# Kernel tuning notes

Hardware: AMD Instinct MI355X
Metric: run time of the kernel (lower is better)

The kernel has to match this reference:

```python
import jax, jax.numpy as jnp
import numpy as np

N, G, E, D, H = 50000, 1000, 400000, 128, 256


def _sample_negatives(edge_index, batch, rng):
    # Vectorized equivalent of the torch per-edge loop: for each positive edge,
    # draw a dst in the same graph as src, excluding src itself and src's
    # existing neighbors, via 8 rounds of rejection sampling.
    src = edge_index[0]
    counts = np.bincount(batch, minlength=G)
    starts = np.concatenate([[0], np.cumsum(counts)[:-1]])
    g = batch[src]
    edge_keys = np.unique(edge_index[0].astype(np.int64) * N + edge_index[1])
    dst = src.copy()
    valid = np.zeros(E, dtype=bool)
    for _ in range(8):
        cand = starts[g] + rng.integers(0, counts[g])
        ok = (cand != src) & ~np.isin(src.astype(np.int64) * N + cand, edge_keys)
        take = ok & ~valid
        dst = np.where(take, cand, dst)
        valid |= ok
    fallback = starts[g] + (src - starts[g] + 1) % counts[g]  # deterministic in-graph node != src (when graph>1)
    dst = np.where(valid, dst, fallback)
    return np.stack([src, dst]).astype(np.int64)


def setup_inputs() -> dict:
    rng = np.random.default_rng(0)
    batch = np.sort(rng.integers(0, G, size=N)).astype(np.int64)  # contiguous graph ids
    counts = np.bincount(batch, minlength=G)
    starts = np.concatenate([[0], np.cumsum(counts)[:-1]])
    src = rng.integers(0, N, size=E)
    gsrc = batch[src]
    dst = starts[gsrc] + rng.integers(0, counts[gsrc])  # same-graph positive edges
    edge_index = np.stack([src, dst]).astype(np.int64)
    neg_edge_index = _sample_negatives(edge_index, batch, rng)

    key = jax.random.key(0)
    ks = jax.random.split(key, 4)
    x = jax.random.normal(ks[0], (N, D), jnp.float32)
    w1 = jax.random.normal(ks[1], (2 * D, H), jnp.float32) / np.sqrt(2 * D)
    w2 = jax.random.normal(ks[2], (H, H // 2), jnp.float32) / np.sqrt(H)
    w3 = jax.random.normal(ks[3], (H // 2, 1), jnp.float32) / np.sqrt(H // 2)
    return {
        "x": x,
        "edge_index": jnp.asarray(edge_index),
        "batch": jnp.asarray(batch),
        "neg_edge_index": jnp.asarray(neg_edge_index),
        "w1": w1, "b1": jnp.zeros((H,), jnp.float32),
        "g1": jnp.ones((H,), jnp.float32), "be1": jnp.zeros((H,), jnp.float32),
        "w2": w2, "b2": jnp.zeros((H // 2,), jnp.float32),
        "g2": jnp.ones((H // 2,), jnp.float32), "be2": jnp.zeros((H // 2,), jnp.float32),
        "w3": w3, "b3": jnp.zeros((1,), jnp.float32),
    }


def _layernorm(h, g, b, eps=1e-5):
    m = jnp.mean(h, axis=-1, keepdims=True)
    v = jnp.mean(jnp.square(h - m), axis=-1, keepdims=True)
    return (h - m) * jax.lax.rsqrt(v + eps) * g + b


def _edge_mlp(feat, w1, b1, g1, be1, w2, b2, g2, be2, w3, b3):
    h = jax.nn.relu(_layernorm(feat @ w1 + b1, g1, be1))
    h = jax.nn.relu(_layernorm(h @ w2 + b2, g2, be2))
    return jax.nn.sigmoid(h @ w3 + b3)


def reference(x, edge_index, batch, neg_edge_index, w1, b1, g1, be1, w2, b2, g2, be2, w3, b3):
    # batch is consumed by the (setup-time) negative sampler; kept for signature fidelity.
    all_idx = jnp.concatenate([edge_index, neg_edge_index], axis=1)  # [2, 2E]
    feat = jnp.concatenate([x[all_idx[0]], x[all_idx[1]]], axis=-1)  # [2E, 2D]
    pred = _edge_mlp(feat, w1, b1, g1, be1, w2, b2, g2, be2, w3, b3)  # [2E, 1]
    num_pos = edge_index.shape[1]
    num_neg = neg_edge_index.shape[1]
    labels = jnp.concatenate(
        [jnp.ones((num_pos, 1), pred.dtype), jnp.zeros((num_neg, 1), pred.dtype)], axis=0
    )
    return pred, labels
```

## Files before the change

### kernel.cpp

```cpp
#include <hip/hip_runtime.h>
#include <math.h>
#include <stdint.h>

#define NN    50000
#define EPOS  400000
#define ROWS  800000
#define DIM   128
#define D2    256
#define H1C   256
#define H2C   128
#define MT    64
#define NTH   512

typedef __bf16 bf16;
typedef __bf16 bf16x8 __attribute__((ext_vector_type(8)));
typedef __bf16 bf16x4 __attribute__((ext_vector_type(4)));
typedef float  f32x4  __attribute__((ext_vector_type(4)));

#define XB_N   (NN*DIM)
#define W1F_E  XB_N
#define W1F_N  (H1C*D2)
#define W2F_E  (XB_N + W1F_N)
#define W2F_N  (H2C*H1C)
#define WS_NEEDED ((size_t)(XB_N + W1F_N + W2F_N) * 2)

#define AOFF  0
#define SCR   32768
#define SCR2  34816
#define CFOFF 35840
#define SMEM_BYTES 40960

__device__ __forceinline__ void gll16(const void* g, void* l) {
    __builtin_amdgcn_global_load_lds(
        (const __attribute__((address_space(1))) void*)g,
        (__attribute__((address_space(3))) void*)l, 16, 0, 0);
}

__global__ void preconv(const float* __restrict__ x, const float* __restrict__ w1,
                        const float* __restrict__ w2, bf16* __restrict__ ws,
                        float* __restrict__ out) {
    int gi = blockIdx.x * 256 + threadIdx.x;
    if (gi < ROWS) out[ROWS + gi] = (gi < EPOS) ? 1.f : 0.f;
    int i = gi;
    if (i < XB_N) { ws[i] = (bf16)x[i]; return; }
    i -= XB_N;
    if (i < W1F_N) {
        int j = i & 7, l = (i >> 3) & 63, ct = i >> 9;
        int c = ct >> 4, t = ct & 15;
        int n = t * 16 + (l & 15);
        int k = c * 32 + (l >> 4) * 8 + j;
        ws[W1F_E + i] = (bf16)w1[k * H1C + n];
        return;
    }
    i -= W1F_N;
    if (i < W2F_N) {
        int j = i & 7, l = (i >> 3) & 63, ct = i >> 9;
        int c = ct >> 3, t = ct & 7;
        int n = t * 16 + (l & 15);
        int k = c * 32 + (l >> 4) * 8 + j;
        ws[W2F_E + i] = (bf16)w2[k * H2C + n];
    }
}

__global__ __launch_bounds__(NTH, 4) void lp_mfma11(
    const bf16* __restrict__ xb, const bf16* __restrict__ w1f, const bf16* __restrict__ w2f,
    const int*  __restrict__ ei, const int* __restrict__ nei,
    const float* __restrict__ b1, const float* __restrict__ g1, const float* __restrict__ be1,
    const float* __restrict__ b2, const float* __restrict__ g2, const float* __restrict__ be2,
    const float* __restrict__ w3, const float* __restrict__ b3,
    float* __restrict__ out)
{
    extern __shared__ char smem[];
    const int tid  = threadIdx.x;
    const int lane = tid & 63;
    const int w    = tid >> 6;
    const int wm   = w >> 2;
    const int wn   = w & 3;
    const int gr0  = blockIdx.x * MT;
    const int l15  = lane & 15;
    const int l4   = lane >> 4;

    #pragma unroll
    for (int ii = 0; ii < 4; ++ii) {
        const int i = w * 4 + ii;
        uint32_t doff = (uint32_t)(i << 10) + (uint32_t)(lane << 4);
        uint32_t loff = doff ^ (((doff >> 9) & 7u) << 4);
        int row = loff >> 9;
        int inb = loff & 511;
        int gr  = gr0 + row;
        int node;
        if (inb < 256) { node = (gr < EPOS) ? ei[gr]        : nei[gr - EPOS]; }
        else           { node = (gr < EPOS) ? ei[EPOS + gr] : nei[gr]; inb -= 256; }
        gll16((const char*)xb + (((size_t)node) << 8) + inb, smem + AOFF + (i << 10));
    }

    for (int i = tid; i < 1280; i += NTH) {
        float v;
        if      (i < 256)  v = b1[i];
        else if (i < 512)  v = g1[i - 256];
        else if (i < 768)  v = be1[i - 512];
        else if (i < 896)  v = b2[i - 768];
        else if (i < 1024) v = g2[i - 896];
        else if (i < 1152) v = be2[i - 1024];
        else               v = w3[i - 1152];
        *(float*)(smem + CFOFF + i * 4) = v;
    }

    uint32_t abase[2], asw[2];
    #pragma unroll
    for (int mi = 0; mi < 2; ++mi) {
        int row = (wm << 5) + (mi << 4) + l15;
        abase[mi] = (uint32_t)row << 9;
        asw[mi]   = (uint32_t)(row & 7) << 4;
    }
    const uint32_t koff  = (uint32_t)l4 << 4;
    const uint32_t c1off = ((uint32_t)wn << 8) + ((uint32_t)l4 << 4);
    const uint32_t c2off = ((uint32_t)wn << 7) + ((uint32_t)l4 << 4);

    __syncthreads();

    f32x4 acc1s[2][4];
    #pragma unroll
    for (int ni = 0; ni < 4; ++ni) {
        f32x4 bias = *(const f32x4*)(smem + CFOFF + c1off + (ni << 6));
        acc1s[0][ni] = bias; acc1s[1][ni] = bias;
    }
    const bf16* bp1 = w1f + (wn << 11) + (lane << 3);
    #pragma unroll
    for (int c = 0; c < 8; ++c) {
        bf16x8 af[2];
        #pragma unroll
        for (int mi = 0; mi < 2; ++mi)
            af[mi] = *(const bf16x8*)(smem + AOFF + ((abase[mi] + ((uint32_t)c << 6) + koff) ^ asw[mi]));
        #pragma unroll
        for (int ni = 0; ni < 4; ++ni) {
            bf16x8 bfr = *(const bf16x8*)(bp1 + (c << 13) + (ni << 9));
            #pragma unroll
            for (int mi = 0; mi < 2; ++mi)
                acc1s[mi][ni] = __builtin_amdgcn_mfma_f32_16x16x32_bf16(
                    bfr, af[mi], acc1s[mi][ni], 0, 0, 0);
        }
    }

    #pragma unroll
    for (int mi = 0; mi < 2; ++mi) {
        float s1 = 0.f, s2 = 0.f;
        #pragma unroll
        for (int ni = 0; ni < 4; ++ni)
            #pragma unroll
            for (int j = 0; j < 4; ++j) {
                float v = acc1s[mi][ni][j];
                s1 += v; s2 += v * v;
            }
        s1 += __shfl_xor(s1, 16); s1 += __shfl_xor(s1, 32);
        s2 += __shfl_xor(s2, 16); s2 += __shfl_xor(s2, 32);
        if (l4 == 0) {
            int row = (wm << 5) + (mi << 4) + l15;
            *(float2*)(smem + SCR + (row << 5) + (wn << 3)) = make_float2(s1, s2);
        }
    }
    __syncthreads();

    #pragma unroll
    for (int mi = 0; mi < 2; ++mi) {
        int row = (wm << 5) + (mi << 4) + l15;
        f32x4 p0 = *(const f32x4*)(smem + SCR + (row << 5));
        f32x4 p1 = *(const f32x4*)(smem + SCR + (row << 5) + 16);
        float s1 = p0[0] + p0[2] + p1[0] + p1[2];
        float s2 = p0[1] + p0[3] + p1[1] + p1[3];
        float mean = s1 * (1.f / 256.f);
        float var  = s2 * (1.f / 256.f) - mean * mean;
        float rstd = rsqrtf(var + 1e-5f);
        #pragma unroll
        for (int ni = 0; ni < 4; ++ni) {
            f32x4 gv  = *(const f32x4*)(smem + CFOFF + 1024 + c1off + (ni << 6));
            f32x4 bev = *(const f32x4*)(smem + CFOFF + 2048 + c1off + (ni << 6));
            bf16x4 hb;
            #pragma unroll
            for (int j = 0; j < 4; ++j) {
                float h = (acc1s[mi][ni][j] - mean) * rstd * gv[j] + bev[j];
                hb[j] = (bf16)fmaxf(h, 0.f);
            }
            uint32_t byte = ((uint32_t)row << 9) + ((uint32_t)wn << 7) + ((uint32_t)ni << 5) + ((uint32_t)l4 << 3);
            byte ^= ((byte >> 9) & 7u) << 4;
            *(bf16x4*)(smem + AOFF + byte) = hb;
        }
    }
    __syncthreads();

    f32x4 acc2s[2][2];
    #pragma unroll
    for (int ni = 0; ni < 2; ++ni) {
        f32x4 bias = *(const f32x4*)(smem + CFOFF + 3072 + c2off + (ni << 6));
        acc2s[0][ni] = bias; acc2s[1][ni] = bias;
    }
    const bf16* bp2 = w2f + (wn << 10) + (lane << 3);
    #pragma unroll
    for (int c = 0; c < 8; ++c) {
        bf16x8 a2[2];
        #pragma unroll
        for (int mi = 0; mi < 2; ++mi)
            a2[mi] = *(const bf16x8*)(smem + AOFF + ((abase[mi] + ((uint32_t)c << 6) + koff) ^ asw[mi]));
        #pragma unroll
        for (int ni = 0; ni < 2; ++ni) {
            bf16x8 b2r = *(const bf16x8*)(bp2 + (c << 12) + (ni << 9));
            #pragma unroll
            for (int mi = 0; mi < 2; ++mi)
                acc2s[mi][ni] = __builtin_amdgcn_mfma_f32_16x16x32_bf16(
                    b2r, a2[mi], acc2s[mi][ni], 0, 0, 0);
        }
    }

    #pragma unroll
    for (int mi = 0; mi < 2; ++mi) {
        float s1 = 0.f, s2 = 0.f;
        #pragma unroll
        for (int ni = 0; ni < 2; ++ni)
            #pragma unroll
            for (int j = 0; j < 4; ++j) {
                float v = acc2s[mi][ni][j];
                s1 += v; s2 += v * v;
            }
        s1 += __shfl_xor(s1, 16); s1 += __shfl_xor(s1, 32);
        s2 += __shfl_xor(s2, 16); s2 += __shfl_xor(s2, 32);
        if (l4 == 0) {
            int row = (wm << 5) + (mi << 4) + l15;
            *(float2*)(smem + SCR + (row << 5) + (wn << 3)) = make_float2(s1, s2);
        }
    }
    __syncthreads();

    #pragma unroll
    for (int mi = 0; mi < 2; ++mi) {
        int row = (wm << 5) + (mi << 4) + l15;
        f32x4 p0 = *(const f32x4*)(smem + SCR + (row << 5));
        f32x4 p1 = *(const f32x4*)(smem + SCR + (row << 5) + 16);
        float s1 = p0[0] + p0[2] + p1[0] + p1[2];
        float s2 = p0[1] + p0[3] + p1[1] + p1[3];
        float mean = s1 * (1.f / 128.f);
        float var  = s2 * (1.f / 128.f) - mean * mean;
        float rstd = rsqrtf(var + 1e-5f);
        float zp = 0.f;
        #pragma unroll
        for (int ni = 0; ni < 2; ++ni) {
            f32x4 gv  = *(const f32x4*)(smem + CFOFF + 3584 + c2off + (ni << 6));
            f32x4 bev = *(const f32x4*)(smem + CFOFF + 4096 + c2off + (ni << 6));
            f32x4 wv  = *(const f32x4*)(smem + CFOFF + 4608 + c2off + (ni << 6));
            #pragma unroll
            for (int j = 0; j < 4; ++j) {
                float h = (acc2s[mi][ni][j] - mean) * rstd * gv[j] + bev[j];
                h = fmaxf(h, 0.f);
                zp += h * wv[j];
            }
        }
        zp += __shfl_xor(zp, 16); zp += __shfl_xor(zp, 32);
        if (l4 == 0)
            *(float*)(smem + SCR2 + (row << 4) + (wn << 2)) = zp;
    }
    __syncthreads();

    if (wn == 0) {
        const float b3s = b3[0];
        #pragma unroll
        for (int mi = 0; mi < 2; ++mi) {
            int row = (wm << 5) + (mi << 4) + l15;
            if (l4 == 0) {
                f32x4 zv = *(const f32x4*)(smem + SCR2 + (row << 4));
                float z = zv[0] + zv[1] + zv[2] + zv[3] + b3s;
                out[gr0 + row] = 1.f / (1.f + expf(-z));
            }
        }
    }
}

#define TILE  32
#define PAD   264
__global__ __launch_bounds__(256, 4) void lp_fused(
    const float* __restrict__ x, const int* __restrict__ ei, const int* __restrict__ nei,
    const float* __restrict__ w1, const float* __restrict__ b1,
    const float* __restrict__ g1, const float* __restrict__ be1,
    const float* __restrict__ w2, const float* __restrict__ b2,
    const float* __restrict__ g2, const float* __restrict__ be2,
    const float* __restrict__ w3, const float* __restrict__ b3,
    float* __restrict__ out)
{
    __shared__ float lds[TILE][PAD];
    const int t = threadIdx.x, e = t >> 3, jg = t & 7;
    const int row = blockIdx.x * TILE + e;
    {
        int src, dst;
        if (row < EPOS) { src = ei[row];         dst = ei[EPOS + row]; }
        else            { src = nei[row - EPOS]; dst = nei[row]; }
        const float* base = (jg < 4) ? (x + src * DIM + jg * 32) : (x + dst * DIM + (jg - 4) * 32);
        const float4* b4 = (const float4*)base;
        #pragma unroll
        for (int s = 0; s < 8; ++s) *(float4*)&lds[e][jg * 32 + s * 4] = b4[s];
    }
    __syncthreads();
    float acc[32];
    #pragma unroll
    for (int i = 0; i < 32; ++i) acc[i] = 0.f;
    const int j0 = jg * 32;
    for (int k4 = 0; k4 < D2 / 4; ++k4) {
        float4 a4 = *(const float4*)&lds[e][k4 * 4];
        float av[4] = {a4.x, a4.y, a4.z, a4.w};
        #pragma unroll
        for (int kk = 0; kk < 4; ++kk) {
            const float a = av[kk];
            const float4* wr = (const float4*)(w1 + (k4 * 4 + kk) * H1C + j0);
            #pragma unroll
            for (int ii = 0; ii < 8; ++ii) {
                float4 wv = wr[ii];
                acc[ii*4+0] += a*wv.x; acc[ii*4+1] += a*wv.y; acc[ii*4+2] += a*wv.z; acc[ii*4+3] += a*wv.w;
            }
        }
    }
    float s1 = 0.f, s2 = 0.f;
    #pragma unroll
    for (int i = 0; i < 32; ++i) { float h = acc[i] + b1[j0+i]; acc[i] = h; s1 += h; s2 += h*h; }
    #pragma unroll
    for (int m = 1; m < 8; m <<= 1) { s1 += __shfl_xor(s1, m, 8); s2 += __shfl_xor(s2, m, 8); }
    float mean = s1 * (1.f/256.f), var = s2 * (1.f/256.f) - mean*mean, rstd = rsqrtf(var + 1e-5f);
    __syncthreads();
    #pragma unroll
    for (int i = 0; i < 32; ++i)
        lds[e][j0+i] = fmaxf((acc[i]-mean)*rstd*g1[j0+i]+be1[j0+i], 0.f);
    __syncthreads();
    float acc2[16];
    #pragma unroll
    for (int i = 0; i < 16; ++i) acc2[i] = 0.f;
    const int q0 = jg * 16;
    for (int k4 = 0; k4 < H1C / 4; ++k4) {
        float4 a4 = *(const float4*)&lds[e][k4 * 4];
        float av[4] = {a4.x, a4.y, a4.z, a4.w};
        #pragma unroll
        for (int kk = 0; kk < 4; ++kk) {
            const float a = av[kk];
            const float4* wr = (const float4*)(w2 + (k4 * 4 + kk) * H2C + q0);
            #pragma unroll
            for (int ii = 0; ii < 4; ++ii) {
                float4 wv = wr[ii];
                acc2[ii*4+0] += a*wv.x; acc2[ii*4+1] += a*wv.y; acc2[ii*4+2] += a*wv.z; acc2[ii*4+3] += a*wv.w;
            }
        }
    }
    s1 = 0.f; s2 = 0.f;
    #pragma unroll
    for (int i = 0; i < 16; ++i) { float h = acc2[i] + b2[q0+i]; acc2[i] = h; s1 += h; s2 += h*h; }
    #pragma unroll
    for (int m = 1; m < 8; m <<= 1) { s1 += __shfl_xor(s1, m, 8); s2 += __shfl_xor(s2, m, 8); }
    mean = s1 * (1.f/128.f); var = s2 * (1.f/128.f) - mean*mean; rstd = rsqrtf(var + 1e-5f);
    float zp = 0.f;
    #pragma unroll
    for (int i = 0; i < 16; ++i) {
        float h = fmaxf((acc2[i]-mean)*rstd*g2[q0+i]+be2[q0+i], 0.f);
        zp += h * w3[q0+i];
    }
    #pragma unroll
    for (int m = 1; m < 8; m <<= 1) zp += __shfl_xor(zp, m, 8);
    if (jg == 0) out[row] = 1.f / (1.f + expf(-(zp + b3[0])));
    if (jg == 1) out[ROWS + row] = (row < EPOS) ? 1.f : 0.f;
}

extern "C" void kernel_launch(void* const* d_in, const int* in_sizes, int n_in,
                              void* d_out, int out_size, void* d_ws, size_t ws_size,
                              hipStream_t stream) {
    const float* x   = (const float*)d_in[0];
    const int*   ei  = (const int*)d_in[1];
    const int*   nei = (const int*)d_in[3];
    const float* w1  = (const float*)d_in[4];
    const float* b1  = (const float*)d_in[5];
    const float* g1  = (const float*)d_in[6];
    const float* be1 = (const float*)d_in[7];
    const float* w2  = (const float*)d_in[8];
    const float* b2  = (const float*)d_in[9];
    const float* g2  = (const float*)d_in[10];
    const float* be2 = (const float*)d_in[11];
    const float* w3  = (const float*)d_in[12];
    const float* b3  = (const float*)d_in[13];
    float* out = (float*)d_out;

    if (ws_size >= WS_NEEDED) {
        bf16* ws = (bf16*)d_ws;
        const int total = XB_N + W1F_N + W2F_N;
        hipLaunchKernelGGL(preconv, dim3((total + 255) / 256), dim3(256), 0, stream,
                           x, w1, w2, ws, out);
        hipFuncSetAttribute((const void*)lp_mfma11,
                            hipFuncAttributeMaxDynamicSharedMemorySize, SMEM_BYTES);
        hipLaunchKernelGGL(lp_mfma11, dim3(ROWS / MT), dim3(NTH), SMEM_BYTES, stream,
                           ws, ws + W1F_E, ws + W2F_E, ei, nei,
                           b1, g1, be1, b2, g2, be2, w3, b3, out);
    } else {
        hipLaunchKernelGGL(lp_fused, dim3(ROWS / TILE), dim3(256), 0, stream,
                           x, ei, nei, w1, b1, g1, be1, w2, b2, g2, be2, w3, b3, out);
    }
}
```

Measured before the change: 270.0 us.

## Precompute per-node first-layer projections and gather them per edge

The first linear layer is split as x[src]@W1a + x[dst]@W1b. A new node_gemm kernel computes both halves for all 50k nodes once (Y of size N×512 in bf16). The edge kernel then gathers and adds the two 256-wide projections before LayerNorm, skipping the per-edge 256×256 GEMM. The cost is an extra kernel, a 51 MB bf16 intermediate, and doubled gather bytes per edge (1 KB vs 512 B). The path only runs when the workspace is large enough, otherwise it falls back to the old kernel.

```diff
diff --git a/kernel.cpp b/kernel.cpp
--- a/kernel.cpp
+++ b/kernel.cpp
@@ -18,23 +18,327 @@
 typedef float  f32x4  __attribute__((ext_vector_type(4)));
 
 #define XB_N   (NN*DIM)
-#define W1F_E  XB_N
-#define W1F_N  (H1C*D2)
-#define W2F_E  (XB_N + W1F_N)
+#define WAF_E  XB_N
+#define WAF_N  (128*512)
+#define W2F_E  (WAF_E + WAF_N)
 #define W2F_N  (H2C*H1C)
-#define WS_NEEDED ((size_t)(XB_N + W1F_N + W2F_N) * 2)
+#define Y_E    (W2F_E + W2F_N)
+#define Y_N    (NN*512)
+#define WS1_NEEDED ((size_t)(W2F_E + W2F_N) * 2)
+#define WS2_NEEDED ((size_t)(Y_E + Y_N) * 2)
+
+__device__ __forceinline__ void gll16(const void* g, void* l) {
+    __builtin_amdgcn_global_load_lds(
+        (const __attribute__((address_space(1))) void*)g,
+        (__attribute__((address_space(3))) void*)l, 16, 0, 0);
+}
+
+__global__ void preconv2(const float* __restrict__ x, const float* __restrict__ w1,
+                         const float* __restrict__ w2, bf16* __restrict__ ws,
+                         float* __restrict__ out) {
+    int gi = blockIdx.x * 256 + threadIdx.x;
+    if (gi < ROWS) out[ROWS + gi] = (gi < EPOS) ? 1.f : 0.f;
+    int i = gi;
+    if (i < XB_N) { ws[i] = (bf16)x[i]; return; }
+    i -= XB_N;
+    if (i < WAF_N) {
+        int j = i & 7, l = (i >> 3) & 63, ct = i >> 9;
+        int c = ct >> 5, t = ct & 31;
+        int np = t * 16 + (l & 15);
+        int k  = c * 32 + (l >> 4) * 8 + j;
+        float v = (np < 256) ? w1[k * H1C + np] : w1[(128 + k) * H1C + (np - 256)];
+        ws[WAF_E + i] = (bf16)v;
+        return;
+    }
+    i -= WAF_N;
+    if (i < W2F_N) {
+        int j = i & 7, l = (i >> 3) & 63, ct = i >> 9;
+        int c = ct >> 3, t = ct & 7;
+        int n = t * 16 + (l & 15);
+        int k = c * 32 + (l >> 4) * 8 + j;
+        ws[W2F_E + i] = (bf16)w2[k * H2C + n];
+    }
+}
+
+__global__ __launch_bounds__(512, 4) void node_gemm(
+    const bf16* __restrict__ xb, const bf16* __restrict__ waf,
+    const float* __restrict__ b1, bf16* __restrict__ Y)
+{
+    __shared__ char smem[16384];
+    const int tid  = threadIdx.x;
+    const int lane = tid & 63;
+    const int w    = tid >> 6;
+    const int wm   = w >> 2;
+    const int wn   = w & 3;
+    const int n0   = blockIdx.x * 64;
+    const int l15  = lane & 15;
+    const int l4   = lane >> 4;
+
+    #pragma unroll
+    for (int ii = 0; ii < 2; ++ii) {
+        const int i = w * 2 + ii;
+        uint32_t doff = (uint32_t)(i << 10) + (uint32_t)(lane << 4);
+        uint32_t loff = doff ^ (((doff >> 8) & 7u) << 4);
+        int row  = loff >> 8;
+        int inb  = loff & 255;
+        int node = n0 + row; if (node >= NN) node = NN - 1;
+        gll16((const char*)xb + ((size_t)node << 8) + inb, smem + (i << 10));
+    }
+    __syncthreads();
+
+    f32x4 acc[2][8] = {};
+    const bf16* bp = waf + (wn << 12) + (lane << 3);
+    uint32_t abase[2], asw[2];
+    #pragma unroll
+    for (int mi = 0; mi < 2; ++mi) {
+        int row = (wm << 5) + (mi << 4) + l15;
+        abase[mi] = (uint32_t)row << 8;
+        asw[mi]   = (uint32_t)(row & 7) << 4;
+    }
+    #pragma unroll
+    for (int c = 0; c < 4; ++c) {
+        bf16x8 af[2];
+        #pragma unroll
+        for (int mi = 0; mi < 2; ++mi)
+            af[mi] = *(const bf16x8*)(smem + ((abase[mi] + ((uint32_t)c << 6) + ((uint32_t)l4 << 4)) ^ asw[mi]));
+        #pragma unroll
+        for (int ni = 0; ni < 8; ++ni) {
+            bf16x8 bfr = *(const bf16x8*)(bp + (c << 14) + (ni << 9));
+            #pragma unroll
+            for (int mi = 0; mi < 2; ++mi)
+                acc[mi][ni] = __builtin_amdgcn_mfma_f32_16x16x32_bf16(
+                    bfr, af[mi], acc[mi][ni], 0, 0, 0);
+        }
+    }
+
+    #pragma unroll
+    for (int mi = 0; mi < 2; ++mi) {
+        int node = n0 + (wm << 5) + (mi << 4) + l15;
+        if (node >= NN) continue;
+        #pragma unroll
+        for (int ni = 0; ni < 8; ++ni) {
+            int col = (wn << 7) + (ni << 4) + (l4 << 2);
+            f32x4 a = acc[mi][ni];
+            if (wn < 2) {
+                f32x4 bv = *(const f32x4*)(b1 + col);
+                a[0] += bv[0]; a[1] += bv[1]; a[2] += bv[2]; a[3] += bv[3];
+            }
+            bf16x4 ob;
+            #pragma unroll
+            for (int j = 0; j < 4; ++j) ob[j] = (bf16)a[j];
+            *(bf16x4*)(Y + ((size_t)node << 9) + col) = ob;
+        }
+    }
+}
+
+#define SOFF  0
+#define DOFF  32768
+#define BSCR  65536
+#define BSCR2 67584
+#define BCF   68608
+#define BSMEM 72704
+
+__global__ __launch_bounds__(NTH, 4) void lp_edge(
+    const bf16* __restrict__ Y, const bf16* __restrict__ w2f,
+    const int*  __restrict__ ei, const int* __restrict__ nei,
+    const float* __restrict__ g1, const float* __restrict__ be1,
+    const float* __restrict__ b2, const float* __restrict__ g2, const float* __restrict__ be2,
+    const float* __restrict__ w3, const float* __restrict__ b3,
+    float* __restrict__ out)
+{
+    extern __shared__ char smem[];
+    const int tid  = threadIdx.x;
+    const int lane = tid & 63;
+    const int w    = tid >> 6;
+    const int wm   = w >> 2;
+    const int wn   = w & 3;
+    const int gr0  = blockIdx.x * MT;
+    const int l15  = lane & 15;
+    const int l4   = lane >> 4;
+
+    #pragma unroll
+    for (int ii = 0; ii < 8; ++ii) {
+        const int i = w * 8 + ii;
+        const int u = i & 31;
+        const int half = i >> 5;
+        uint32_t doff = (uint32_t)(u << 10) + (uint32_t)(lane << 4);
+        uint32_t loff = doff ^ (((doff >> 9) & 7u) << 4);
+        int row = loff >> 9;
+        int inb = loff & 511;
+        int gr  = gr0 + row;
+        int node = (half == 0) ? ((gr < EPOS) ? ei[gr]        : nei[gr - EPOS])
+                               : ((gr < EPOS) ? ei[EPOS + gr] : nei[gr]);
+        gll16((const char*)Y + ((size_t)node << 10) + (half << 9) + inb,
+              smem + (half ? DOFF : SOFF) + (u << 10));
+    }
+
+    for (int i = tid; i < 1024; i += NTH) {
+        float v;
+        if      (i < 256) v = g1[i];
+        else if (i < 512) v = be1[i - 256];
+        else if (i < 640) v = b2[i - 512];
+        else if (i < 768) v = g2[i - 640];
+        else if (i < 896) v = be2[i - 768];
+        else              v = w3[i - 896];
+        *(float*)(smem + BCF + i * 4) = v;
+    }
+
+    uint32_t abase[2], asw[2];
+    #pragma unroll
+    for (int mi = 0; mi < 2; ++mi) {
+        int row = (wm << 5) + (mi << 4) + l15;
+        abase[mi] = (uint32_t)row << 9;
+        asw[mi]   = (uint32_t)(row & 7) << 4;
+    }
+    const uint32_t koff  = (uint32_t)l4 << 4;
+    const uint32_t c1off = ((uint32_t)wn << 8) + ((uint32_t)l4 << 4);
+    const uint32_t c2off = ((uint32_t)wn << 7) + ((uint32_t)l4 << 4);
+
+    __syncthreads();
+
+    f32x4 pv[2][4];
+    #pragma unroll
+    for (int mi = 0; mi < 2; ++mi) {
+        float s1 = 0.f, s2 = 0.f;
+        int row = (wm << 5) + (mi << 4) + l15;
+        uint32_t rsw = (uint32_t)(row & 7) << 4;
+        #pragma unroll
+        for (int ni = 0; ni < 4; ++ni) {
+            uint32_t byte = (((uint32_t)row << 9) + ((uint32_t)wn << 7) + ((uint32_t)ni << 5) + ((uint32_t)l4 << 3)) ^ rsw;
+            bf16x4 sv = *(const bf16x4*)(smem + SOFF + byte);
+            bf16x4 dv = *(const bf16x4*)(smem + DOFF + byte);
+            f32x4 v;
+            #pragma unroll
+            for (int j = 0; j < 4; ++j) {
+                v[j] = (float)sv[j] + (float)dv[j];
+                s1 += v[j]; s2 += v[j] * v[j];
+            }
+            pv[mi][ni] = v;
+        }
+        s1 += __shfl_xor(s1, 16); s1 += __shfl_xor(s1, 32);
+        s2 += __shfl_xor(s2, 16); s2 += __shfl_xor(s2, 32);
+        if (l4 == 0)
+            *(float2*)(smem + BSCR + (row << 5) + (wn << 3)) = make_float2(s1, s2);
+    }
+    __syncthreads();
+
+    #pragma unroll
+    for (int mi = 0; mi < 2; ++mi) {
+        int row = (wm << 5) + (mi << 4) + l15;
+        f32x4 p0 = *(const f32x4*)(smem + BSCR + (row << 5));
+        f32x4 p1 = *(const f32x4*)(smem + BSCR + (row << 5) + 16);
+        float s1 = p0[0] + p0[2] + p1[0] + p1[2];
+        float s2 = p0[1] + p0[3] + p1[1] + p1[3];
+        float mean = s1 * (1.f / 256.f);
+        float var  = s2 * (1.f / 256.f) - mean * mean;
+        float rstd = rsqrtf(var + 1e-5f);
+        #pragma unroll
+        for (int ni = 0; ni < 4; ++ni) {
+            f32x4 gv  = *(const f32x4*)(smem + BCF + c1off + (ni << 6));
+            f32x4 bev = *(const f32x4*)(smem + BCF + 1024 + c1off + (ni << 6));
+            bf16x4 hb;
+            #pragma unroll
+            for (int j = 0; j < 4; ++j) {
+                float h = (pv[mi][ni][j] - mean) * rstd * gv[j] + bev[j];
+                hb[j] = (bf16)fmaxf(h, 0.f);
+            }
+            uint32_t byte = ((uint32_t)row << 9) + ((uint32_t)wn << 7) + ((uint32_t)ni << 5) + ((uint32_t)l4 << 3);
+            byte ^= ((byte >> 9) & 7u) << 4;
+            *(bf16x4*)(smem + SOFF + byte) = hb;
+        }
+    }
+    __syncthreads();
+
+    f32x4 acc2s[2][2];
+    #pragma unroll
+    for (int ni = 0; ni < 2; ++ni) {
+        f32x4 bias = *(const f32x4*)(smem + BCF + 2048 + c2off + (ni << 6));
+        acc2s[0][ni] = bias; acc2s[1][ni] = bias;
+    }
+    const bf16* bp2 = w2f + (wn << 10) + (lane << 3);
+    #pragma unroll
+    for (int c = 0; c < 8; ++c) {
+        bf16x8 a2[2];
+        #pragma unroll
+        for (int mi = 0; mi < 2; ++mi)
+            a2[mi] = *(const bf16x8*)(smem + SOFF + ((abase[mi] + ((uint32_t)c << 6) + koff) ^ asw[mi]));
+        #pragma unroll
+        for (int ni = 0; ni < 2; ++ni) {
+            bf16x8 b2r = *(const bf16x8*)(bp2 + (c << 12) + (ni << 9));
+            #pragma unroll
+            for (int mi = 0; mi < 2; ++mi)
+                acc2s[mi][ni] = __builtin_amdgcn_mfma_f32_16x16x32_bf16(
+                    b2r, a2[mi], acc2s[mi][ni], 0, 0, 0);
+        }
+    }
+
+    #pragma unroll
+    for (int mi = 0; mi < 2; ++mi) {
+        float s1 = 0.f, s2 = 0.f;
+        #pragma unroll
+        for (int ni = 0; ni < 2; ++ni)
+            #pragma unroll
+            for (int j = 0; j < 4; ++j) {
+                float v = acc2s[mi][ni][j];
+                s1 += v; s2 += v * v;
+            }
+        s1 += __shfl_xor(s1, 16); s1 += __shfl_xor(s1, 32);
+        s2 += __shfl_xor(s2, 16); s2 += __shfl_xor(s2, 32);
+        if (l4 == 0) {
+            int row = (wm << 5) + (mi << 4) + l15;
+            *(float2*)(smem + BSCR + (row << 5) + (wn << 3)) = make_float2(s1, s2);
+        }
+    }
+    __syncthreads();
+
+    #pragma unroll
+    for (int mi = 0; mi < 2; ++mi) {
+        int row = (wm << 5) + (mi << 4) + l15;
+        f32x4 p0 = *(const f32x4*)(smem + BSCR + (row << 5));
+        f32x4 p1 = *(const f32x4*)(smem + BSCR + (row << 5) + 16);
+        float s1 = p0[0] + p0[2] + p1[0] + p1[2];
+        float s2 = p0[1] + p0[3] + p1[1] + p1[3];
+        float mean = s1 * (1.f / 128.f);
+        float var  = s2 * (1.f / 128.f) - mean * mean;
+        float rstd = rsqrtf(var + 1e-5f);
+        float zp = 0.f;
+        #pragma unroll
+        for (int ni = 0; ni < 2; ++ni) {
+            f32x4 gv  = *(const f32x4*)(smem + BCF + 2560 + c2off + (ni << 6));
+            f32x4 bev = *(const f32x4*)(smem + BCF + 3072 + c2off + (ni << 6));
+            f32x4 wv  = *(const f32x4*)(smem + BCF + 3584 + c2off + (ni << 6));
+            #pragma unroll
+            for (int j = 0; j < 4; ++j) {
+                float h = (acc2s[mi][ni][j] - mean) * rstd * gv[j] + bev[j];
+                h = fmaxf(h, 0.f);
+                zp += h * wv[j];
+            }
+        }
+        zp += __shfl_xor(zp, 16); zp += __shfl_xor(zp, 32);
+        if (l4 == 0)
+            *(float*)(smem + BSCR2 + (row << 4) + (wn << 2)) = zp;
+    }
+    __syncthreads();
+
+    if (wn == 0) {
+        const float b3s = b3[0];
+        #pragma unroll
+        for (int mi = 0; mi < 2; ++mi) {
+            int row = (wm << 5) + (mi << 4) + l15;
+            if (l4 == 0) {
+                f32x4 zv = *(const f32x4*)(smem + BSCR2 + (row << 4));
+                float z = zv[0] + zv[1] + zv[2] + zv[3] + b3s;
+                out[gr0 + row] = 1.f / (1.f + expf(-z));
+            }
+        }
+    }
+}
 
 #define AOFF  0
 #define SCR   32768
 #define SCR2  34816
 #define CFOFF 35840
 #define SMEM_BYTES 40960
-
-__device__ __forceinline__ void gll16(const void* g, void* l) {
-    __builtin_amdgcn_global_load_lds(
-        (const __attribute__((address_space(1))) void*)g,
-        (__attribute__((address_space(3))) void*)l, 16, 0, 0);
-}
 
 __global__ void preconv(const float* __restrict__ x, const float* __restrict__ w1,
                         const float* __restrict__ w2, bf16* __restrict__ ws,
@@ -44,15 +348,15 @@
     int i = gi;
     if (i < XB_N) { ws[i] = (bf16)x[i]; return; }
     i -= XB_N;
-    if (i < W1F_N) {
+    if (i < WAF_N) {
         int j = i & 7, l = (i >> 3) & 63, ct = i >> 9;
         int c = ct >> 4, t = ct & 15;
         int n = t * 16 + (l & 15);
         int k = c * 32 + (l >> 4) * 8 + j;
-        ws[W1F_E + i] = (bf16)w1[k * H1C + n];
+        ws[WAF_E + i] = (bf16)w1[k * H1C + n];
         return;
     }
-    i -= W1F_N;
+    i -= WAF_N;
     if (i < W2F_N) {
         int j = i & 7, l = (i >> 3) & 63, ct = i >> 9;
         int c = ct >> 3, t = ct & 7;
@@ -93,7 +397,6 @@
         else           { node = (gr < EPOS) ? ei[EPOS + gr] : nei[gr]; inb -= 256; }
         gll16((const char*)xb + (((size_t)node) << 8) + inb, smem + AOFF + (i << 10));
     }
-
     for (int i = tid; i < 1280; i += NTH) {
         float v;
         if      (i < 256)  v = b1[i];
@@ -105,7 +408,6 @@
         else               v = w3[i - 1152];
         *(float*)(smem + CFOFF + i * 4) = v;
     }
-
     uint32_t abase[2], asw[2];
     #pragma unroll
     for (int mi = 0; mi < 2; ++mi) {
@@ -116,7 +418,6 @@
     const uint32_t koff  = (uint32_t)l4 << 4;
     const uint32_t c1off = ((uint32_t)wn << 8) + ((uint32_t)l4 << 4);
     const uint32_t c2off = ((uint32_t)wn << 7) + ((uint32_t)l4 << 4);
-
     __syncthreads();
 
     f32x4 acc1s[2][4];
@@ -141,7 +442,6 @@
                     bfr, af[mi], acc1s[mi][ni], 0, 0, 0);
         }
     }
-
     #pragma unroll
     for (int mi = 0; mi < 2; ++mi) {
         float s1 = 0.f, s2 = 0.f;
@@ -160,7 +460,6 @@
         }
     }
     __syncthreads();
-
     #pragma unroll
     for (int mi = 0; mi < 2; ++mi) {
         int row = (wm << 5) + (mi << 4) + l15;
@@ -210,7 +509,6 @@
                     b2r, a2[mi], acc2s[mi][ni], 0, 0, 0);
         }
     }
-
     #pragma unroll
     for (int mi = 0; mi < 2; ++mi) {
         float s1 = 0.f, s2 = 0.f;
@@ -229,7 +527,6 @@
         }
     }
     __syncthreads();
-
     #pragma unroll
     for (int mi = 0; mi < 2; ++mi) {
         int row = (wm << 5) + (mi << 4) + l15;
@@ -258,7 +555,6 @@
             *(float*)(smem + SCR2 + (row << 4) + (wn << 2)) = zp;
     }
     __syncthreads();
-
     if (wn == 0) {
         const float b3s = b3[0];
         #pragma unroll
@@ -380,15 +676,27 @@
     const float* b3  = (const float*)d_in[13];
     float* out = (float*)d_out;
 
-    if (ws_size >= WS_NEEDED) {
+    if (ws_size >= WS2_NEEDED) {
         bf16* ws = (bf16*)d_ws;
-        const int total = XB_N + W1F_N + W2F_N;
+        const int total = XB_N + WAF_N + W2F_N;
+        hipLaunchKernelGGL(preconv2, dim3((total + 255) / 256), dim3(256), 0, stream,
+                           x, w1, w2, ws, out);
+        hipLaunchKernelGGL(node_gemm, dim3((NN + 63) / 64), dim3(512), 0, stream,
+                           ws, ws + WAF_E, b1, ws + Y_E);
+        hipFuncSetAttribute((const void*)lp_edge,
+                            hipFuncAttributeMaxDynamicSharedMemorySize, BSMEM);
+        hipLaunchKernelGGL(lp_edge, dim3(ROWS / MT), dim3(NTH), BSMEM, stream,
+                           ws + Y_E, ws + W2F_E, ei, nei,
+                           g1, be1, b2, g2, be2, w3, b3, out);
+    } else if (ws_size >= WS1_NEEDED) {
+        bf16* ws = (bf16*)d_ws;
+        const int total = XB_N + WAF_N + W2F_N;
         hipLaunchKernelGGL(preconv, dim3((total + 255) / 256), dim3(256), 0, stream,
                            x, w1, w2, ws, out);
         hipFuncSetAttribute((const void*)lp_mfma11,
                             hipFuncAttributeMaxDynamicSharedMemorySize, SMEM_BYTES);
         hipLaunchKernelGGL(lp_mfma11, dim3(ROWS / MT), dim3(NTH), SMEM_BYTES, stream,
-                           ws, ws + W1F_E, ws + W2F_E, ei, nei,
+                           ws, ws + WAF_E, ws + W2F_E, ei, nei,
                            b1, g1, be1, b2, g2, be2, w3, b3, out);
     } else {
         hipLaunchKernelGGL(lp_fused, dim3(ROWS / TILE), dim3(256), 0, stream,
```

After: 289.6 us. 7.3% more time.
